# Performance work log

Measured on AMD Instinct MI355X. Metric: run time of the kernel, lower is better.

## Reference

```python
import jax, jax.numpy as jnp
import numpy as np

N_P, N_W, F_IN = 512, 3584, 256
H1, O1 = 8, 32
H2, O2 = 8, 256
BATCH = 1024
NEG_SLOPE = 0.2


def _xavier(key, shape):
    fan_in, fan_out = shape[-2], shape[-1]
    lim = jnp.sqrt(6.0 / (fan_in + fan_out))
    return jax.random.uniform(key, shape, jnp.float32, -lim, lim)


def setup_inputs() -> dict:
    key = jax.random.key(0)
    ks = jax.random.split(key, 16)
    return {
        "input": jax.random.uniform(ks[0], (BATCH, N_W), jnp.float32),
        "pern_feature": jax.random.normal(ks[1], (N_P, F_IN), jnp.float32),
        "word_feature": jax.random.normal(ks[2], (N_W, F_IN), jnp.float32),
        "w1": _xavier(ks[3], (H1, F_IN, O1)),
        "a_src1": _xavier(ks[4], (H1, O1, 1)),
        "a_dst1": _xavier(ks[5], (H1, O1, 1)),
        "b1": jnp.zeros((O1,), jnp.float32),
        "w2": _xavier(ks[6], (H2, F_IN, O2)),
        "a_src2": _xavier(ks[7], (H2, F_IN, 1)),
        "a_dst2": _xavier(ks[8], (H2, F_IN, 1)),
        "b2": jnp.zeros((O2,), jnp.float32),
        "W_fc": _xavier(ks[9], (O2, 5)),
        "b_fc": jnp.zeros((5,), jnp.float32),
        "pern_adj": jax.random.randint(ks[10], (N_P, N_P), 0, 2, jnp.int32),
        "word_pern_adj": jax.random.randint(ks[11], (N_P + N_W, N_P + N_W), 0, 2, jnp.int32),
    }


def gat(h, adj, w, a_src, a_dst, bias):
    # h: [N, f_in], adj: [N, N] int, w: [H, f_in, f_out]
    h_prime = jnp.einsum('nf,hfo->hno', h, w)          # [H, N, O]
    t = jnp.tanh(h_prime)
    s_src = jnp.einsum('hno,hoi->hn', t, a_src)        # [H, N]
    s_dst = jnp.einsum('hno,hoi->hn', t, a_dst)        # [H, N]
    attn = s_src[:, :, None] + s_dst[:, None, :]       # [H, N, N]
    attn = jnp.where(attn >= 0, attn, NEG_SLOPE * attn)  # leaky_relu
    attn = jnp.where(adj[None, :, :] > 0, attn, -jnp.inf)
    attn = jax.nn.softmax(attn, axis=-1)
    out = jnp.einsum('hnm,hmo->hno', attn, h_prime)    # [H, N, O]
    return out + bias


def reference(input, pern_feature, word_feature, w1, a_src1, a_dst1, b1,
              w2, a_src2, a_dst2, b2, W_fc, b_fc, pern_adj, word_pern_adj):
    n_p = pern_feature.shape[0]
    # GAT 1 over personality graph
    h1 = gat(pern_feature, pern_adj, w1, a_src1, a_dst1, b1)       # [H1, n_p, O1]
    hiddn_pp = jnp.transpose(h1, (1, 0, 2)).reshape(n_p, -1)        # [n_p, H1*O1]
    hiddn_pp = jax.nn.elu(hiddn_pp)
    # dropout is identity in eval mode
    hiddn_wp = jnp.concatenate([word_feature, hiddn_pp], axis=0)    # [N, 256]
    h2 = gat(hiddn_wp, word_pern_adj, w2, a_src2, a_dst2, b2)       # [H2, N, O2]
    hiddn_wp2 = h2.mean(axis=0)                                     # [N, O2]
    hiddn_w = hiddn_wp2[:word_feature.shape[0], :]                  # [n_w, O2]
    x = (input @ hiddn_w) / input.sum(axis=1, keepdims=True)        # [B, O2]
    return x @ W_fc + b_fc                                          # [B, 5]
```

## Files before the change

### kernel.cpp

```cpp
#include <hip/hip_runtime.h>
#include <hip/hip_bf16.h>
#include <math.h>

#define NP 512
#define NW 3584
#define NT 4096
#define FIN 256
#define H1 8
#define O1 32
#define H2 8
#define O2 256
#define NEG 0.2f

typedef __attribute__((ext_vector_type(8))) short bf16x8;
typedef __attribute__((ext_vector_type(4))) float f32x4;
typedef unsigned long long u64;

__device__ __forceinline__ unsigned short f2bf(float f) {
    unsigned u = __float_as_uint(f);
    unsigned r = (u + 0x7FFF + ((u >> 16) & 1)) >> 16;
    return (unsigned short)r;
}
__device__ __forceinline__ float rflf(float x) {
    return __uint_as_float(__builtin_amdgcn_readfirstlane(__float_as_uint(x)));
}

__global__ __launch_bounds__(256) void k_prep(
    const float* __restrict__ wf, const float* __restrict__ pf,
    const float* __restrict__ w1, const float* __restrict__ a_src1,
    const float* __restrict__ a_dst1, const float* __restrict__ w2,
    const float* __restrict__ b2, const float* __restrict__ W_fc,
    const float* __restrict__ a_src2, const float* __restrict__ a_dst2,
    const int* __restrict__ wp_adj,
    unsigned short* __restrict__ abf, unsigned short* __restrict__ btbf,
    float* __restrict__ hp1, float* __restrict__ ss1, float* __restrict__ sd1,
    unsigned* __restrict__ maskT, float* __restrict__ cvec,
    float* __restrict__ wtab)
{
    __shared__ float tile[64][65];
    __shared__ float feat[2][FIN];
    __shared__ float red[4][5];
    int blk = blockIdx.x;
    int t = threadIdx.x;
    if (blk < 896) {
        int idx4 = blk * 256 + t;
        float4 x = ((const float4*)wf)[idx4];
        ushort4 y;
        y.x = f2bf(x.x); y.y = f2bf(x.y); y.z = f2bf(x.z); y.w = f2bf(x.w);
        ((ushort4*)abf)[idx4] = y;
    } else if (blk < 1152) {
        int n0 = (blk - 896) * 2;
        feat[0][t] = pf[n0 * FIN + t];
        feat[1][t] = pf[(n0 + 1) * FIN + t];
        __syncthreads();
        int h = t >> 5, o = t & 31;
        float acc0 = 0.f, acc1 = 0.f;
        const float* wcol = w1 + h * FIN * O1 + o;
        #pragma unroll 4
        for (int f = 0; f < FIN; f++) {
            float w = wcol[f * O1];
            acc0 += feat[0][f] * w;
            acc1 += feat[1][f] * w;
        }
        hp1[n0 * 256 + t] = acc0;
        hp1[(n0 + 1) * 256 + t] = acc1;
        float as = a_src1[h * O1 + o];
        float ad = a_dst1[h * O1 + o];
        float accs[2] = {acc0, acc1};
        #pragma unroll
        for (int i = 0; i < 2; i++) {
            float th = tanhf(accs[i]);
            float vs = th * as, vd = th * ad;
            #pragma unroll
            for (int off = 1; off < 32; off <<= 1) {
                vs += __shfl_xor(vs, off);
                vd += __shfl_xor(vd, off);
            }
            if (o == 0) { ss1[h * NP + n0 + i] = vs; sd1[h * NP + n0 + i] = vd; }
        }
    } else if (blk < 1280) {
        int blk2 = blk - 1152;
        int h = blk2 >> 4;
        int f0 = ((blk2 >> 2) & 3) * 64;
        int o0 = (blk2 & 3) * 64;
        #pragma unroll
        for (int rr = 0; rr < 16; rr++) {
            int f = rr * 4 + (t >> 6);
            int o = t & 63;
            tile[f][o] = w2[((size_t)(h * FIN + f0 + f)) * O2 + o0 + o];
        }
        __syncthreads();
        #pragma unroll
        for (int rr = 0; rr < 16; rr++) {
            int o = rr * 4 + (t >> 6);
            int f = t & 63;
            btbf[((size_t)(h * O2 + o0 + o)) * FIN + f0 + f] = f2bf(tile[f][o]);
        }
    } else if (blk < 2176) {
        int w = t >> 6, l = t & 63;
        int r = (blk - 1280) * 4 + w;
        const int4* row = (const int4*)(wp_adj + (size_t)r * NT);
        for (int c4 = 0; c4 < 16; c4++) {
            int4 x = row[c4 * 64 + l];
            u64 nib = (u64)((x.x != 0 ? 1 : 0) | (x.y != 0 ? 2 : 0) |
                            (x.z != 0 ? 4 : 0) | (x.w != 0 ? 8 : 0));
            u64 v = nib << (4 * (l & 15));
            v |= __shfl_xor(v, 1);
            v |= __shfl_xor(v, 2);
            v |= __shfl_xor(v, 4);
            v |= __shfl_xor(v, 8);
            if ((l & 15) == 0) {
                int qw = c4 * 4 + (l >> 4);
                maskT[(size_t)(2 * qw) * NW + r]     = (unsigned)v;
                maskT[(size_t)(2 * qw + 1) * NW + r] = (unsigned)(v >> 32);
            }
        }
    } else if (blk == 2176) {
        float v[5];
        #pragma unroll
        for (int j = 0; j < 5; j++) v[j] = b2[t] * W_fc[t * 5 + j];
        #pragma unroll
        for (int off = 1; off < 64; off <<= 1)
            #pragma unroll
            for (int j = 0; j < 5; j++) v[j] += __shfl_xor(v[j], off);
        int w = t >> 6, l = t & 63;
        if (l == 0) { for (int j = 0; j < 5; j++) red[w][j] = v[j]; }
        __syncthreads();
        if (t == 0)
            for (int j = 0; j < 5; j++) cvec[j] = red[0][j] + red[1][j] + red[2][j] + red[3][j];
    } else {
        int h = blk - 2177;
        int o = t;
        float* dst = wtab + ((size_t)h * O2 + o) * 8;
        float4 d0 = {a_src2[h * O2 + o], a_dst2[h * O2 + o], W_fc[o * 5], W_fc[o * 5 + 1]};
        float4 d1 = {W_fc[o * 5 + 2], W_fc[o * 5 + 3], W_fc[o * 5 + 4], 0.f};
        *(float4*)dst = d0;
        *(float4*)(dst + 4) = d1;
    }
}

__global__ __launch_bounds__(256) void k_gat1_attn(
    const int* __restrict__ adj, const float* __restrict__ hp1,
    const float* __restrict__ ss1, const float* __restrict__ sd1,
    float* __restrict__ g1acc, float* __restrict__ g1den)
{
    __shared__ float af[256];
    __shared__ float p[8][256];
    __shared__ float den8[8];
    int t = threadIdx.x;
    int b = blockIdx.x;
    int n = b >> 1, mh = b & 1;
    int mbase = mh * 256;
    af[t] = adj[n * NP + mbase + t] > 0 ? 1.0f : 0.0f;
    __syncthreads();
    #pragma unroll
    for (int r = 0; r < 8; r++) {
        int idx = r * 256 + t;
        int h = idx >> 8, m = idx & 255;
        float e = ss1[h * NP + n] + sd1[h * NP + mbase + m];
        e = fmaxf(e, NEG * e);
        p[h][m] = af[m] * __expf(e);
    }
    __syncthreads();
    int w = t >> 6, l = t & 63;
    #pragma unroll
    for (int hh = 0; hh < 2; hh++) {
        int h = w + hh * 4;
        float s = 0;
        #pragma unroll
        for (int k = 0; k < 4; k++) s += p[h][l + 64 * k];
        #pragma unroll
        for (int off = 1; off < 64; off <<= 1) s += __shfl_xor(s, off);
        if (l == 0) den8[h] = s;
    }
    __syncthreads();
    int h = t >> 5;
    float acc0 = 0.f, acc1 = 0.f;
    #pragma unroll 8
    for (int m = 0; m < 256; m += 2) {
        acc0 += p[h][m]     * hp1[(mbase + m) * 256 + t];
        acc1 += p[h][m + 1] * hp1[(mbase + m + 1) * 256 + t];
    }
    g1acc[((size_t)mh * NP + n) * 256 + t] = acc0 + acc1;
    if (t < 8) g1den[((size_t)mh * NP + n) * 8 + t] = den8[t];
}

__global__ __launch_bounds__(256) void k_gat1_comb(
    const float* __restrict__ g1acc, const float* __restrict__ g1den,
    const float* __restrict__ b1, unsigned short* __restrict__ abf)
{
    int n = blockIdx.x, t = threadIdx.x;
    int h = t >> 5, o = t & 31;
    float acc = g1acc[(size_t)n * 256 + t] + g1acc[((size_t)NP + n) * 256 + t];
    float den = g1den[(size_t)n * 8 + h] + g1den[((size_t)NP + n) * 8 + h];
    float r = acc / den + b1[o];
    r = r > 0.f ? r : expm1f(r);
    abf[(size_t)(NW + n) * FIN + t] = f2bf(r);
}

__global__ __launch_bounds__(256) void k_gemm_hp2(
    const unsigned short* __restrict__ abf, const unsigned short* __restrict__ btbf,
    const float* __restrict__ wtab, float* __restrict__ gpart)
{
    __shared__ unsigned short As[64][264];
    int b = blockIdx.x;
    int h = b & 7, mt = b >> 3;
    int t = threadIdx.x;
    int w = t >> 6, l = t & 63;
    int m0 = mt * 64;
    {
        int row = t >> 5;
        int col8 = (t & 31) * 8;
        #pragma unroll
        for (int u = 0; u < 8; u++)
            *(bf16x8*)(&As[u * 8 + row][col8]) =
                *(const bf16x8*)(abf + (size_t)(m0 + u * 8 + row) * FIN + col8);
    }
    __syncthreads();
    int n0 = w * 64;
    int lr = l & 15, lq = l >> 4;
    const unsigned short* bbase = btbf + h * O2 * FIN;
    f32x4 acc[4][4];
    #pragma unroll
    for (int i = 0; i < 4; i++)
        #pragma unroll
        for (int j = 0; j < 4; j++) acc[i][j] = (f32x4){0.f, 0.f, 0.f, 0.f};
    #pragma unroll
    for (int k = 0; k < FIN; k += 32) {
        bf16x8 a[4], bf[4];
        int kc = k + lq * 8;
        #pragma unroll
        for (int j = 0; j < 4; j++)
            bf[j] = *(const bf16x8*)(bbase + (size_t)(n0 + j * 16 + lr) * FIN + kc);
        #pragma unroll
        for (int i = 0; i < 4; i++)
            a[i] = *(const bf16x8*)(&As[i * 16 + lr][kc]);
        #pragma unroll
        for (int i = 0; i < 4; i++)
            #pragma unroll
            for (int j = 0; j < 4; j++)
                acc[i][j] = __builtin_amdgcn_mfma_f32_16x16x32_bf16(bf[j], a[i], acc[i][j], 0, 0, 0);
    }
    const float* wt = wtab + (size_t)h * O2 * 8;
    float* base = gpart + ((size_t)h * 4 + w) * NT * 8;
    #pragma unroll
    for (int i = 0; i < 4; i++) {
        float s[7] = {0,0,0,0,0,0,0};
        #pragma unroll
        for (int j = 0; j < 4; j++) {
            #pragma unroll
            for (int r = 0; r < 4; r++) {
                float x = acc[i][j][r];
                float ex = __expf(2.0f * x);
                float th = 1.0f - 2.0f * __builtin_amdgcn_rcpf(ex + 1.0f);
                const float* wp = wt + (size_t)(n0 + j * 16 + lq * 4 + r) * 8;
                float4 wa = *(const float4*)wp;
                float4 wb = *(const float4*)(wp + 4);
                s[0] += th * wa.x;
                s[1] += th * wa.y;
                s[2] += x * wa.z;
                s[3] += x * wa.w;
                s[4] += x * wb.x;
                s[5] += x * wb.y;
                s[6] += x * wb.z;
            }
        }
        #pragma unroll
        for (int q = 0; q < 7; q++) {
            s[q] += __shfl_xor(s[q], 16);
            s[q] += __shfl_xor(s[q], 32);
        }
        if (lq == 0) {
            int m = m0 + i * 16 + lr;
            float* dst = base + (size_t)m * 8;
            #pragma unroll
            for (int q = 0; q < 7; q++) dst[q] = s[q];
        }
    }
}

__global__ __launch_bounds__(256) void k_comb_hp2(
    const float* __restrict__ gpart,
    float* __restrict__ Etab, float* __restrict__ Eptab, float* __restrict__ T)
{
    int idx = blockIdx.x * 256 + threadIdx.x;
    float s[7] = {0,0,0,0,0,0,0};
    #pragma unroll
    for (int sl = 0; sl < 4; sl++) {
        const float* p = gpart + (((size_t)(idx >> 12) * 4 + sl) * NT + (idx & (NT - 1))) * 8;
        #pragma unroll
        for (int q = 0; q < 7; q++) s[q] += p[q];
    }
    Etab[idx]  = __expf(s[0]);
    Eptab[idx] = __expf(NEG * s[0]);
    float4 t0 = {__expf(s[1]), __expf(NEG * s[1]), 1.0f, s[2]};
    float4 t1 = {s[3], s[4], s[5], s[6]};
    *(float4*)(T + (size_t)idx * 8)     = t0;
    *(float4*)(T + (size_t)idx * 8 + 4) = t1;
}

__global__ __launch_bounds__(256) void k_gat2_attn(
    const unsigned* __restrict__ maskT, const float* __restrict__ Etab,
    const float* __restrict__ Eptab, const float* __restrict__ T,
    float* __restrict__ part)
{
    __shared__ unsigned pw[32 * 32];
    int t = threadIdx.x;
    int w = t >> 6, l = t & 63;
    int b = blockIdx.x;
    int nb = b % 112;
    int h  = (b / 112) & 7;
    int c  = b / 896;
    int rbase = nb * 32;
    #pragma unroll
    for (int u = 0; u < 4; u++) {
        int idx = u * 256 + t;
        int wd = idx >> 5, row = idx & 31;
        pw[idx] = maskT[(size_t)(c * 32 + wd) * NW + rbase + row];
    }
    __syncthreads();
    int n0 = rbase + w * 8;
    float E[8], Ep[8];
    #pragma unroll
    for (int i = 0; i < 8; i++) {
        int r = h * NT + n0 + i;
        E[i]  = rflf(Etab[r]);
        Ep[i] = rflf(Eptab[r]);
    }
    float den[8] = {0,0,0,0,0,0,0,0};
    float num[8][5] = {{0}};
    const float* Th = T + ((size_t)h * NT + c * 1024) * 8;
    int lsh = l & 31;
    int wdh = l >> 5;
    const unsigned* mbase = pw + w * 8;
    #pragma unroll 2
    for (int q = 0; q < 16; q++) {
        const float* tp = Th + (size_t)(q * 64 + l) * 8;
        f32x4 t0 = *(const f32x4*)tp;
        f32x4 t1 = *(const f32x4*)(tp + 4);
        int wd = q * 2 + wdh;
        uint4 ma = *(const uint4*)(mbase + wd * 32);
        uint4 mb = *(const uint4*)(mbase + wd * 32 + 4);
        unsigned wv[8] = {ma.x, ma.y, ma.z, ma.w, mb.x, mb.y, mb.z, mb.w};
        #pragma unroll
        for (int i = 0; i < 8; i++) {
            float bm = (float)((wv[i] >> lsh) & 1u);
            float pa = t0.x * E[i];
            float pb = t0.y * Ep[i];
            float pp = fmaxf(pa, pb) * bm;
            den[i] += pp;
            num[i][0] = fmaf(pp, t0.w, num[i][0]);
            num[i][1] = fmaf(pp, t1.x, num[i][1]);
            num[i][2] = fmaf(pp, t1.y, num[i][2]);
            num[i][3] = fmaf(pp, t1.z, num[i][3]);
            num[i][4] = fmaf(pp, t1.w, num[i][4]);
        }
    }
    #pragma unroll
    for (int i = 0; i < 8; i++) {
        float v[6];
        v[0] = den[i];
        #pragma unroll
        for (int j = 0; j < 5; j++) v[1 + j] = num[i][j];
        #pragma unroll
        for (int off = 1; off < 32; off <<= 1)
            #pragma unroll
            for (int k = 0; k < 6; k++) v[k] += __shfl_xor(v[k], off);
        if ((l & 31) == 0) {
            float* dst = part + ((((size_t)c * NW + n0 + i) * 8 + h) * 2 + (l >> 5)) * 8;
            #pragma unroll
            for (int k = 0; k < 6; k++) dst[k] = v[k];
        }
    }
}

__global__ __launch_bounds__(256) void k_gat2_comb(const float* __restrict__ part,
                                                   float* __restrict__ hf) {
    int idx = blockIdx.x * 256 + threadIdx.x;
    int n = idx >> 3, h = idx & 7;
    float den = 0, num[5] = {0,0,0,0,0};
    #pragma unroll
    for (int cc = 0; cc < 4; cc++) {
        #pragma unroll
        for (int s = 0; s < 2; s++) {
            const float* p = part + ((((size_t)cc * NW + n) * 8 + h) * 2 + s) * 8;
            float4 a = *(const float4*)p;
            float4 bq = *(const float4*)(p + 4);
            den += a.x;
            num[0] += a.y; num[1] += a.z; num[2] += a.w;
            num[3] += bq.x; num[4] += bq.y;
        }
    }
    float inv = 1.0f / (den * 8.0f);
    float v[5];
    #pragma unroll
    for (int j = 0; j < 5; j++) v[j] = num[j] * inv;
    #pragma unroll
    for (int off = 1; off < 8; off <<= 1)
        #pragma unroll
        for (int j = 0; j < 5; j++) v[j] += __shfl_xor(v[j], off);
    if (h == 0) {
        #pragma unroll
        for (int j = 0; j < 5; j++) hf[n * 5 + j] = v[j];
    }
}

__global__ __launch_bounds__(256) void k_final(
    const float* __restrict__ input, const float* __restrict__ hf,
    const float* __restrict__ cvec, const float* __restrict__ b_fc,
    float* __restrict__ out)
{
    int b = blockIdx.x, t = threadIdx.x;
    const float4* row4 = (const float4*)(input + (size_t)b * NW);
    const float4* hf4 = (const float4*)hf;
    float s = 0.f, a[5] = {0.f, 0.f, 0.f, 0.f, 0.f};
    for (int idx = t; idx < NW / 4; idx += 256) {
        float4 x = row4[idx];
        float f[20];
        #pragma unroll
        for (int q = 0; q < 5; q++) *(float4*)(f + 4 * q) = hf4[idx * 5 + q];
        s += x.x + x.y + x.z + x.w;
        #pragma unroll
        for (int j = 0; j < 5; j++)
            a[j] += x.x * f[j] + x.y * f[5 + j] + x.z * f[10 + j] + x.w * f[15 + j];
    }
    #pragma unroll
    for (int off = 1; off < 64; off <<= 1) {
        s += __shfl_xor(s, off);
        #pragma unroll
        for (int j = 0; j < 5; j++) a[j] += __shfl_xor(a[j], off);
    }
    __shared__ float red[4][6];
    int w = t >> 6, l = t & 63;
    if (l == 0) { red[w][0] = s; for (int j = 0; j < 5; j++) red[w][j + 1] = a[j]; }
    __syncthreads();
    if (t < 5) {
        float st = red[0][0] + red[1][0] + red[2][0] + red[3][0];
        float aj = red[0][t + 1] + red[1][t + 1] + red[2][t + 1] + red[3][t + 1];
        out[b * 5 + t] = aj / st + cvec[t] + b_fc[t];
    }
}

extern "C" void kernel_launch(void* const* d_in, const int* in_sizes, int n_in,
                              void* d_out, int out_size, void* d_ws, size_t ws_size,
                              hipStream_t stream) {
    const float* input   = (const float*)d_in[0];
    const float* pf      = (const float*)d_in[1];
    const float* wf      = (const float*)d_in[2];
    const float* w1      = (const float*)d_in[3];
    const float* a_src1  = (const float*)d_in[4];
    const float* a_dst1  = (const float*)d_in[5];
    const float* b1      = (const float*)d_in[6];
    const float* w2      = (const float*)d_in[7];
    const float* a_src2  = (const float*)d_in[8];
    const float* a_dst2  = (const float*)d_in[9];
    const float* b2      = (const float*)d_in[10];
    const float* W_fc    = (const float*)d_in[11];
    const float* b_fc    = (const float*)d_in[12];
    const int* pern_adj  = (const int*)d_in[13];
    const int* wp_adj    = (const int*)d_in[14];
    float* out = (float*)d_out;

    char* ws = (char*)d_ws;
    unsigned short* abf    = (unsigned short*)(ws);
    unsigned short* btbf   = (unsigned short*)(ws + 2097152);
    float*          hp1    = (float*)(ws + 3145728);
    float*          ss1    = (float*)(ws + 3670016);
    float*          sd1    = (float*)(ws + 3686400);
    float*          Etab   = (float*)(ws + 3833856);
    float*          Eptab  = (float*)(ws + 3964928);
    float*          T      = (float*)(ws + 4096000);
    float*          hf     = (float*)(ws + 5144576);
    float*          cvec   = (float*)(ws + 5216256);
    unsigned*       maskT  = (unsigned*)(ws + 5216512);
    float*          gpart  = (float*)(ws + 7051520);
    float*          g1acc  = (float*)(ws + 11245824);
    float*          g1den  = (float*)(ws + 12294400);
    float*          part   = (float*)(ws + 12582912);
    float*          wtab   = (float*)(ws + 26214400);

    k_prep<<<2185, 256, 0, stream>>>(wf, pf, w1, a_src1, a_dst1, w2, b2, W_fc,
                                     a_src2, a_dst2, wp_adj,
                                     abf, btbf, hp1, ss1, sd1, maskT, cvec, wtab);
    k_gat1_attn<<<1024, 256, 0, stream>>>(pern_adj, hp1, ss1, sd1, g1acc, g1den);
    k_gat1_comb<<<512, 256, 0, stream>>>(g1acc, g1den, b1, abf);
    k_gemm_hp2<<<512, 256, 0, stream>>>(abf, btbf, wtab, gpart);
    k_comb_hp2<<<128, 256, 0, stream>>>(gpart, Etab, Eptab, T);
    k_gat2_attn<<<3584, 256, 0, stream>>>(maskT, Etab, Eptab, T, part);
    k_gat2_comb<<<112, 256, 0, stream>>>(part, hf);
    k_final<<<1024, 256, 0, stream>>>(input, hf, cvec, b_fc, out);
}
```

Measured before the change: 250.8 us.

## Fuse GAT1 combine into hp2 GEMM and enlarge GAT2 attention tiles

The GAT1 combine step (sum of partials, normalise, bias, ELU, bf16 convert) now runs inside the hp2 GEMM's A-tile load for the personality rows, which removes one kernel launch and the abf round trip. The GAT2 attention kernel now covers 64 rows by 2048 columns per block instead of 32 by 1024, so each wave holds 16 rows and lanes reduce only within groups of 8. This gives more reuse of each T load across rows and a shorter shuffle reduction, at the cost of more registers, fewer blocks (896) and larger partial buffers for the combine step. The workspace offset for wtab is moved to make room for the bigger partial buffer.

```diff
diff --git a/kernel.cpp b/kernel.cpp
--- a/kernel.cpp
+++ b/kernel.cpp
@@ -185,22 +185,11 @@
     if (t < 8) g1den[((size_t)mh * NP + n) * 8 + t] = den8[t];
 }
 
-__global__ __launch_bounds__(256) void k_gat1_comb(
-    const float* __restrict__ g1acc, const float* __restrict__ g1den,
-    const float* __restrict__ b1, unsigned short* __restrict__ abf)
-{
-    int n = blockIdx.x, t = threadIdx.x;
-    int h = t >> 5, o = t & 31;
-    float acc = g1acc[(size_t)n * 256 + t] + g1acc[((size_t)NP + n) * 256 + t];
-    float den = g1den[(size_t)n * 8 + h] + g1den[((size_t)NP + n) * 8 + h];
-    float r = acc / den + b1[o];
-    r = r > 0.f ? r : expm1f(r);
-    abf[(size_t)(NW + n) * FIN + t] = f2bf(r);
-}
-
 __global__ __launch_bounds__(256) void k_gemm_hp2(
     const unsigned short* __restrict__ abf, const unsigned short* __restrict__ btbf,
-    const float* __restrict__ wtab, float* __restrict__ gpart)
+    const float* __restrict__ wtab, const float* __restrict__ g1acc,
+    const float* __restrict__ g1den, const float* __restrict__ b1,
+    float* __restrict__ gpart)
 {
     __shared__ unsigned short As[64][264];
     int b = blockIdx.x;
@@ -208,13 +197,37 @@
     int t = threadIdx.x;
     int w = t >> 6, l = t & 63;
     int m0 = mt * 64;
-    {
+    if (m0 < NW) {
         int row = t >> 5;
         int col8 = (t & 31) * 8;
         #pragma unroll
         for (int u = 0; u < 8; u++)
             *(bf16x8*)(&As[u * 8 + row][col8]) =
                 *(const bf16x8*)(abf + (size_t)(m0 + u * 8 + row) * FIN + col8);
+    } else {
+        int row = t >> 5;
+        int col8 = (t & 31) * 8;
+        int hc = col8 >> 5;
+        #pragma unroll
+        for (int u = 0; u < 8; u++) {
+            int n = m0 + u * 8 + row - NW;
+            float4 a0 = *(const float4*)(g1acc + (size_t)n * 256 + col8);
+            float4 a1 = *(const float4*)(g1acc + (size_t)n * 256 + col8 + 4);
+            float4 c0 = *(const float4*)(g1acc + ((size_t)NP + n) * 256 + col8);
+            float4 c1 = *(const float4*)(g1acc + ((size_t)NP + n) * 256 + col8 + 4);
+            float dn = g1den[(size_t)n * 8 + hc] + g1den[((size_t)NP + n) * 8 + hc];
+            float inv = 1.0f / dn;
+            float vals[8] = {a0.x + c0.x, a0.y + c0.y, a0.z + c0.z, a0.w + c0.w,
+                             a1.x + c1.x, a1.y + c1.y, a1.z + c1.z, a1.w + c1.w};
+            unsigned short us[8];
+            #pragma unroll
+            for (int j = 0; j < 8; j++) {
+                float r = vals[j] * inv + b1[(col8 & 31) + j];
+                r = r > 0.f ? r : expm1f(r);
+                us[j] = f2bf(r);
+            }
+            *(bf16x8*)(&As[u * 8 + row][col8]) = *(bf16x8*)us;
+        }
     }
     __syncthreads();
     int n0 = w * 64;
@@ -304,50 +317,56 @@
     const float* __restrict__ Eptab, const float* __restrict__ T,
     float* __restrict__ part)
 {
-    __shared__ unsigned pw[32 * 32];
+    __shared__ unsigned pw[64 * 64];
     int t = threadIdx.x;
     int w = t >> 6, l = t & 63;
     int b = blockIdx.x;
-    int nb = b % 112;
-    int h  = (b / 112) & 7;
-    int c  = b / 896;
-    int rbase = nb * 32;
-    #pragma unroll
-    for (int u = 0; u < 4; u++) {
+    int nb = b % 56;
+    int h  = (b / 56) & 7;
+    int c  = b / 448;
+    int rbase = nb * 64;
+    #pragma unroll
+    for (int u = 0; u < 16; u++) {
         int idx = u * 256 + t;
-        int wd = idx >> 5, row = idx & 31;
-        pw[idx] = maskT[(size_t)(c * 32 + wd) * NW + rbase + row];
+        int wd = idx >> 6, row = idx & 63;
+        pw[idx] = maskT[(size_t)(c * 64 + wd) * NW + rbase + row];
     }
     __syncthreads();
-    int n0 = rbase + w * 8;
-    float E[8], Ep[8];
-    #pragma unroll
-    for (int i = 0; i < 8; i++) {
+    int n0 = rbase + w * 16;
+    float E[16], Ep[16];
+    #pragma unroll
+    for (int i = 0; i < 16; i++) {
         int r = h * NT + n0 + i;
         E[i]  = rflf(Etab[r]);
         Ep[i] = rflf(Eptab[r]);
     }
-    float den[8] = {0,0,0,0,0,0,0,0};
-    float num[8][5] = {{0}};
-    const float* Th = T + ((size_t)h * NT + c * 1024) * 8;
+    float den[16];
+    float num[16][5];
+    #pragma unroll
+    for (int i = 0; i < 16; i++) {
+        den[i] = 0.f;
+        #pragma unroll
+        for (int j = 0; j < 5; j++) num[i][j] = 0.f;
+    }
+    const float* Th = T + ((size_t)h * NT + c * 2048) * 8;
     int lsh = l & 31;
     int wdh = l >> 5;
-    const unsigned* mbase = pw + w * 8;
-    #pragma unroll 2
-    for (int q = 0; q < 16; q++) {
+    const unsigned* mb0 = pw + w * 16;
+    for (int q = 0; q < 32; q++) {
         const float* tp = Th + (size_t)(q * 64 + l) * 8;
         f32x4 t0 = *(const f32x4*)tp;
         f32x4 t1 = *(const f32x4*)(tp + 4);
-        int wd = q * 2 + wdh;
-        uint4 ma = *(const uint4*)(mbase + wd * 32);
-        uint4 mb = *(const uint4*)(mbase + wd * 32 + 4);
-        unsigned wv[8] = {ma.x, ma.y, ma.z, ma.w, mb.x, mb.y, mb.z, mb.w};
-        #pragma unroll
-        for (int i = 0; i < 8; i++) {
+        const unsigned* mb = mb0 + (q * 2 + wdh) * 64;
+        uint4 ma = *(const uint4*)(mb);
+        uint4 mc = *(const uint4*)(mb + 4);
+        uint4 me = *(const uint4*)(mb + 8);
+        uint4 mg = *(const uint4*)(mb + 12);
+        unsigned wv[16] = {ma.x, ma.y, ma.z, ma.w, mc.x, mc.y, mc.z, mc.w,
+                           me.x, me.y, me.z, me.w, mg.x, mg.y, mg.z, mg.w};
+        #pragma unroll
+        for (int i = 0; i < 16; i++) {
             float bm = (float)((wv[i] >> lsh) & 1u);
-            float pa = t0.x * E[i];
-            float pb = t0.y * Ep[i];
-            float pp = fmaxf(pa, pb) * bm;
+            float pp = fmaxf(t0.x * E[i], t0.y * Ep[i]) * bm;
             den[i] += pp;
             num[i][0] = fmaf(pp, t0.w, num[i][0]);
             num[i][1] = fmaf(pp, t1.x, num[i][1]);
@@ -357,17 +376,17 @@
         }
     }
     #pragma unroll
-    for (int i = 0; i < 8; i++) {
+    for (int i = 0; i < 16; i++) {
         float v[6];
         v[0] = den[i];
         #pragma unroll
         for (int j = 0; j < 5; j++) v[1 + j] = num[i][j];
         #pragma unroll
-        for (int off = 1; off < 32; off <<= 1)
+        for (int off = 1; off < 8; off <<= 1)
             #pragma unroll
             for (int k = 0; k < 6; k++) v[k] += __shfl_xor(v[k], off);
-        if ((l & 31) == 0) {
-            float* dst = part + ((((size_t)c * NW + n0 + i) * 8 + h) * 2 + (l >> 5)) * 8;
+        if ((l & 7) == 0) {
+            float* dst = part + ((((size_t)c * NW + n0 + i) * 8 + h) * 8 + (l >> 3)) * 8;
             #pragma unroll
             for (int k = 0; k < 6; k++) dst[k] = v[k];
         }
@@ -380,10 +399,10 @@
     int n = idx >> 3, h = idx & 7;
     float den = 0, num[5] = {0,0,0,0,0};
     #pragma unroll
-    for (int cc = 0; cc < 4; cc++) {
-        #pragma unroll
-        for (int s = 0; s < 2; s++) {
-            const float* p = part + ((((size_t)cc * NW + n) * 8 + h) * 2 + s) * 8;
+    for (int cc = 0; cc < 2; cc++) {
+        #pragma unroll
+        for (int s = 0; s < 8; s++) {
+            const float* p = part + ((((size_t)cc * NW + n) * 8 + h) * 8 + s) * 8;
             float4 a = *(const float4*)p;
             float4 bq = *(const float4*)(p + 4);
             den += a.x;
@@ -477,16 +496,15 @@
     float*          g1acc  = (float*)(ws + 11245824);
     float*          g1den  = (float*)(ws + 12294400);
     float*          part   = (float*)(ws + 12582912);
-    float*          wtab   = (float*)(ws + 26214400);
+    float*          wtab   = (float*)(ws + 28311552);
 
     k_prep<<<2185, 256, 0, stream>>>(wf, pf, w1, a_src1, a_dst1, w2, b2, W_fc,
                                      a_src2, a_dst2, wp_adj,
                                      abf, btbf, hp1, ss1, sd1, maskT, cvec, wtab);
     k_gat1_attn<<<1024, 256, 0, stream>>>(pern_adj, hp1, ss1, sd1, g1acc, g1den);
-    k_gat1_comb<<<512, 256, 0, stream>>>(g1acc, g1den, b1, abf);
-    k_gemm_hp2<<<512, 256, 0, stream>>>(abf, btbf, wtab, gpart);
+    k_gemm_hp2<<<512, 256, 0, stream>>>(abf, btbf, wtab, g1acc, g1den, b1, gpart);
     k_comb_hp2<<<128, 256, 0, stream>>>(gpart, Etab, Eptab, T);
-    k_gat2_attn<<<3584, 256, 0, stream>>>(maskT, Etab, Eptab, T, part);
+    k_gat2_attn<<<896, 256, 0, stream>>>(maskT, Etab, Eptab, T, part);
     k_gat2_comb<<<112, 256, 0, stream>>>(part, hf);
     k_final<<<1024, 256, 0, stream>>>(input, hf, cvec, b_fc, out);
 }
```

New measurement: 258.0 us. 1.03x slower.
